# Kernel optimization log

Measured on AMD Instinct MI355X. Metric: run time of the kernel, lower is better.

The kernel has to match this reference:

```python
import jax, jax.numpy as jnp
import numpy as np

B, IN_LEN, L = 32, 10, 16384
N_POLY, M_MODES, K_STR, CH, NB = 12, 6, 2, 20, 4


def _legendre_filters():
    # Midpoints of n equal intervals on [-1, 1]
    j = np.arange(N_POLY)
    xs = -1.0 + (2.0 * j + 1.0) / N_POLY
    fr = np.stack([np.polynomial.legendre.Legendre.basis(i)(xs) for i in range(M_MODES)])
    fd = fr * ((2.0 * np.arange(M_MODES) + 1.0) / N_POLY)[:, None]  # decomposition quadrature weights
    return fd[:, None, :].astype(np.float32), fr[:, None, :].astype(np.float32)


def _conv1d(x, w, stride=1):
    return jax.lax.conv_general_dilated(x, w, (stride,), 'VALID',
                                        dimension_numbers=('NCH', 'OIH', 'NCH'))


def setup_inputs() -> dict:
    key = jax.random.key(0)
    ks = jax.random.split(key, 7)
    sc = 0.1
    fd, fr = _legendre_filters()
    return {
        'input':   jax.random.normal(ks[0], (B, IN_LEN, L), jnp.float32),
        'w_first': jax.random.normal(ks[1], (CH, IN_LEN, 3), jnp.float32) * sc,
        'conv_a':  jax.random.normal(ks[2], (NB, CH, CH, 3), jnp.float32) * sc,
        'conv_b':  jax.random.normal(ks[3], (NB, CH, CH, 3), jnp.float32) * sc,
        'lin_m':   jax.random.normal(ks[4], (NB, CH, M_MODES, M_MODES), jnp.float32) * sc,
        'w11':     jax.random.normal(ks[5], (128, CH, 1), jnp.float32) * sc,
        'w_out':   jax.random.normal(ks[6], (1, 128, 1), jnp.float32) * sc,
        'filt_d':  jnp.asarray(fd),
        'filt_r':  jnp.asarray(fr),
    }


def reference(input, w_first, conv_a, conv_b, lin_m, w11, w_out, filt_d, filt_r):
    n, m, kk = N_POLY, M_MODES, K_STR
    s = n // kk                      # conv stride = 6
    nb = conv_a.shape[0]
    RR = (n // kk) * (kk - 1)        # 6
    recept = RR * nb + 1
    rc = 2
    gelu = lambda t: jax.nn.gelu(t, approximate=False)

    b, _, Lin = input.shape
    li = Lin + 2 * recept - 2
    half = n // 2
    r = half - li % half             # circular padding to make strided conv exact
    x = jnp.pad(input, ((0, 0), (0, 0), (recept, recept + r)), mode='wrap')
    x = _conv1d(x, w_first)          # (b, CH, l)
    c = x.shape[1]

    for i in range(nb):
        l = x.shape[-1]
        # local residual branch: conv3 -> gelu -> conv3
        linear_x = _conv1d(gelu(_conv1d(x, conv_a[i])), conv_b[i])  # (b, c, l-4)
        # Legendre decomposition: strided conv per (b,c) signal
        xr = x.reshape(b * c, 1, l)
        Lx = _conv1d(xr, filt_d / kk, stride=s)                     # (b*c, m, ll)
        ll = Lx.shape[-1]
        Lx = Lx.reshape(b, c, m, ll).transpose(0, 2, 1, 3).reshape(b, m * c, ll)
        # grouped 1x1 conv: groups=c consecutive chunks of size m over the (mode-major) channel axis
        Lg = Lx.reshape(b, c, m, ll)
        Lg = jnp.einsum('bgil,goi->bgol', Lg, lin_m[i])
        Lx2 = Lg.reshape(b, m * c, ll)
        Lx2 = Lx2.reshape(b, m, c, ll).transpose(0, 2, 1, 3).reshape(b * c, m, ll) * 2.0
        # conv_transpose1d (stride s, kernel n=2s) via overlap-add of two half-kernels
        y = jnp.einsum('xmt,mk->xtk', Lx2, (filt_r / kk)[:, 0, :])  # (b*c, ll, n)
        p1 = y[..., :s].reshape(b * c, ll * s)
        p2 = y[..., s:].reshape(b * c, ll * s)
        rec = jnp.pad(p1, ((0, 0), (0, s))) + jnp.pad(p2, ((0, 0), (s, 0)))  # (b*c, l)
        rec = rec.reshape(b, c, l)
        x = gelu(rec[:, :, RR:-RR] + linear_x[:, :, RR - rc:-(RR - rc)])

    x = gelu(jnp.einsum('bcl,oc->bol', x, w11[:, :, 0]))
    x = jnp.einsum('bcl,oc->bol', x, w_out[:, :, 0])
    return x[:, :, :-r]
```

## Files before the change

kernel.cpp:

```cpp
#include <hip/hip_runtime.h>
#include <math.h>

#define B_ 32
#define INLEN 10
#define LIN_ 16384
#define NPOLY 12
#define MM 6
#define CH 20
#define NB 4
#define RECEPT 25
#define L0 16434
#define TTILE 252
#define NW 43
#define XS_LEN 264
#define XS_PAD 265
#define GS_LEN 254
#define LXS_PAD 121
#define CCHUNK 5
#define COH 10

__device__ __forceinline__ float gelu_exact(float x) {
    return 0.5f * x * (1.0f + erff(x * 0.70710678118654752440f));
}

__global__ void k_first(const float* __restrict__ in, const float* __restrict__ wf,
                        float* __restrict__ out) {
    int t = blockIdx.x * blockDim.x + threadIdx.x;
    int b = blockIdx.y;
    if (t >= L0) return;
    const float* inb = in + (size_t)b * INLEN * LIN_;
    float xw[INLEN][3];
#pragma unroll
    for (int ci = 0; ci < INLEN; ++ci) {
#pragma unroll
        for (int k = 0; k < 3; ++k) {
            int idx = t + k - RECEPT;
            idx = (idx < 0) ? idx + LIN_ : (idx >= LIN_ ? idx - LIN_ : idx);
            xw[ci][k] = inb[ci * LIN_ + idx];
        }
    }
    float* outb = out + (size_t)b * CH * L0;
#pragma unroll
    for (int co = 0; co < CH; ++co) {
        float acc = 0.f;
#pragma unroll
        for (int ci = 0; ci < INLEN; ++ci)
#pragma unroll
            for (int k = 0; k < 3; ++k)
                acc = fmaf(xw[ci][k], wf[(co * INLEN + ci) * 3 + k], acc);
        outb[(size_t)co * L0 + t] = acc;
    }
}

__global__ __launch_bounds__(512, 2)
void k_block(const float* __restrict__ x, float* __restrict__ xn,
             const float* __restrict__ wA, const float* __restrict__ wB,
             const float* __restrict__ linm, const float* __restrict__ fd,
             const float* __restrict__ fr, int l) {
    const int lout = l - 12;
    const int tid  = threadIdx.x;
    const int t    = tid & 255;
    const int half = __builtin_amdgcn_readfirstlane(tid >> 8);
    const int cob  = half * COH;
    const int t0   = blockIdx.x * TTILE;
    const int b    = blockIdx.y;

    const float* wAh = wA + cob * CH * 3;
    const float* wBh = wB + cob * CH * 3;

    __shared__ float xs[CH][XS_PAD];
    __shared__ float lxs[NW][LXS_PAD];
    __shared__ float lm_s[CH * MM * MM];
    __shared__ float fr_s[MM * NPOLY];

    const float* xb = x + (size_t)b * CH * l;

    for (int i = tid; i < CH * MM * MM; i += 512) lm_s[i] = linm[i];
    for (int i = tid; i < MM * NPOLY; i += 512)   fr_s[i] = fr[i];

    for (int i = tid; i < CH * XS_LEN; i += 512) {
        int c = i / XS_LEN, p = i - c * XS_LEN;
        int gp = t0 + p;
        xs[c][p] = (gp < l) ? xb[(size_t)c * l + gp] : 0.f;
    }
    __syncthreads();

    for (int item = tid; item < NW * CH; item += 512) {
        int wl = item / CH, c = item - wl * CH;
        float xv[NPOLY];
#pragma unroll
        for (int k = 0; k < NPOLY; ++k) xv[k] = xs[c][6 * wl + k];
#pragma unroll
        for (int m = 0; m < MM; ++m) {
            float acc = 0.f;
#pragma unroll
            for (int k = 0; k < NPOLY; ++k)
                acc = fmaf(xv[k], fd[m * NPOLY + k], acc);
            lxs[wl][m * CH + c] = acc * 0.5f;
        }
    }

    float gv[COH];
    if (t < GS_LEN) {
#pragma unroll
        for (int co = 0; co < COH; ++co) gv[co] = 0.f;
#pragma unroll 1
        for (int cig = 0; cig < CH; cig += CCHUNK) {
            float xw[CCHUNK][3];
#pragma unroll
            for (int j = 0; j < CCHUNK; ++j) {
                xw[j][0] = xs[cig + j][t + 4];
                xw[j][1] = xs[cig + j][t + 5];
                xw[j][2] = xs[cig + j][t + 6];
            }
#pragma unroll
            for (int co = 0; co < COH; ++co) {
                float acc = gv[co];
#pragma unroll
                for (int j = 0; j < CCHUNK; ++j)
#pragma unroll
                    for (int k = 0; k < 3; ++k)
                        acc = fmaf(xw[j][k], wAh[(co * CH + cig + j) * 3 + k], acc);
                gv[co] = acc;
            }
        }
#pragma unroll
        for (int co = 0; co < COH; ++co) gv[co] = gelu_exact(gv[co]);
    }
    __syncthreads();

    if (t < GS_LEN) {
#pragma unroll
        for (int co = 0; co < COH; ++co) xs[cob + co][t] = gv[co];
    }

    for (int item = tid; item < NW * CH; item += 512) {
        int wl = item / CH, g = item - wl * CH;
        float iv[MM], ov[MM];
#pragma unroll
        for (int i = 0; i < MM; ++i) iv[i] = lxs[wl][g * MM + i];
#pragma unroll
        for (int o = 0; o < MM; ++o) {
            float acc = 0.f;
#pragma unroll
            for (int i = 0; i < MM; ++i)
                acc = fmaf(iv[i], lm_s[(g * MM + o) * MM + i], acc);
            ov[o] = acc;
        }
#pragma unroll
        for (int o = 0; o < MM; ++o) lxs[wl][g * MM + o] = ov[o];
    }
    __syncthreads();

    if (t < TTILE && t0 + t < lout) {
        const int tp = t;
        float acc[COH];
#pragma unroll
        for (int co = 0; co < COH; ++co) acc[co] = 0.f;
#pragma unroll 1
        for (int cig = 0; cig < CH; cig += CCHUNK) {
            float aw[CCHUNK][3];
#pragma unroll
            for (int j = 0; j < CCHUNK; ++j) {
                aw[j][0] = xs[cig + j][tp];
                aw[j][1] = xs[cig + j][tp + 1];
                aw[j][2] = xs[cig + j][tp + 2];
            }
#pragma unroll
            for (int co = 0; co < COH; ++co) {
                float a = acc[co];
#pragma unroll
                for (int j = 0; j < CCHUNK; ++j)
#pragma unroll
                    for (int k = 0; k < 3; ++k)
                        a = fmaf(aw[j][k], wBh[(co * CH + cig + j) * 3 + k], a);
                acc[co] = a;
            }
        }
        const int r1  = tp % 6;
        const int wl1 = tp / 6 + 1;
        float frA[MM], frB[MM];
#pragma unroll
        for (int m = 0; m < MM; ++m) {
            frA[m] = fr_s[m * NPOLY + r1];
            frB[m] = fr_s[m * NPOLY + r1 + 6];
        }
        float* xnb = xn + (size_t)b * CH * lout + (size_t)cob * lout;
#pragma unroll
        for (int co = 0; co < COH; ++co) {
            float rec = 0.f;
#pragma unroll
            for (int m = 0; m < MM; ++m) {
                rec = fmaf(lxs[wl1][m * CH + cob + co], frA[m], rec);
                rec = fmaf(lxs[wl1 - 1][m * CH + cob + co], frB[m], rec);
            }
            xnb[(size_t)co * lout + t0 + tp] = gelu_exact(acc[co] + rec);
        }
    }
}

__global__ void k_final(const float* __restrict__ x, const float* __restrict__ w11,
                        const float* __restrict__ wout, float* __restrict__ out) {
    int t = blockIdx.x * blockDim.x + threadIdx.x;
    int b = blockIdx.y;
    if (t >= LIN_) return;
    const int l4 = L0 - NB * 12;
    const float* xb = x + (size_t)b * CH * l4;
    float xv[CH];
#pragma unroll
    for (int c = 0; c < CH; ++c) xv[c] = xb[(size_t)c * l4 + t];
    float acc0 = 0.f, acc1 = 0.f, acc2 = 0.f, acc3 = 0.f;
    for (int h = 0; h < 128; h += 4) {
        float hv0 = 0.f, hv1 = 0.f, hv2 = 0.f, hv3 = 0.f;
#pragma unroll
        for (int c = 0; c < CH; ++c) {
            hv0 = fmaf(xv[c], w11[(h + 0) * CH + c], hv0);
            hv1 = fmaf(xv[c], w11[(h + 1) * CH + c], hv1);
            hv2 = fmaf(xv[c], w11[(h + 2) * CH + c], hv2);
            hv3 = fmaf(xv[c], w11[(h + 3) * CH + c], hv3);
        }
        acc0 = fmaf(gelu_exact(hv0), wout[h + 0], acc0);
        acc1 = fmaf(gelu_exact(hv1), wout[h + 1], acc1);
        acc2 = fmaf(gelu_exact(hv2), wout[h + 2], acc2);
        acc3 = fmaf(gelu_exact(hv3), wout[h + 3], acc3);
    }
    out[(size_t)b * LIN_ + t] = (acc0 + acc1) + (acc2 + acc3);
}

extern "C" void kernel_launch(void* const* d_in, const int* in_sizes, int n_in,
                              void* d_out, int out_size, void* d_ws, size_t ws_size,
                              hipStream_t stream) {
    const float* input   = (const float*)d_in[0];
    const float* w_first = (const float*)d_in[1];
    const float* conv_a  = (const float*)d_in[2];
    const float* conv_b  = (const float*)d_in[3];
    const float* lin_m   = (const float*)d_in[4];
    const float* w11     = (const float*)d_in[5];
    const float* w_out   = (const float*)d_in[6];
    const float* filt_d  = (const float*)d_in[7];
    const float* filt_r  = (const float*)d_in[8];
    float* out = (float*)d_out;

    const size_t bufElems = (size_t)B_ * CH * L0;
    float* xA = (float*)d_ws;
    float* xB = xA + bufElems;

    {
        dim3 grid((L0 + 255) / 256, B_);
        k_first<<<grid, 256, 0, stream>>>(input, w_first, xA);
    }

    int l = L0;
    float* cur = xA;
    float* nxt = xB;
    for (int i = 0; i < NB; ++i) {
        int lout  = l - 12;
        int tiles = (lout + TTILE - 1) / TTILE;
        dim3 grid(tiles, B_);
        k_block<<<grid, 512, 0, stream>>>(cur, nxt,
                                          conv_a + i * CH * CH * 3,
                                          conv_b + i * CH * CH * 3,
                                          lin_m + i * CH * MM * MM,
                                          filt_d, filt_r, l);
        float* tswap = cur; cur = nxt; nxt = tswap;
        l = lout;
    }

    {
        dim3 grid((LIN_ + 255) / 256, B_);
        k_final<<<grid, 256, 0, stream>>>(cur, w11, w_out, out);
    }
}
```

Before: 495.3 us.

## Fuse first conv into first block and final MLP into last block

The stem convolution is computed inside the first residual-block kernel from a shared-memory tile of the wrapped input, and the last block kernel applies the 1x1 conv, GELU and output projection itself, splitting the 128 hidden units across the two thread halves. This removes two kernel launches and the global write and re-read of a full 20-channel activation tensor at each end. In exchange the first block recomputes the stem conv on tile halos, and the last block gains extra syncs and a serial 64-hidden loop per thread.

Result: no change. 487.1 us (-1.7%).

```diff
diff --git a/kernel.cpp b/kernel.cpp
--- a/kernel.cpp
+++ b/kernel.cpp
@@ -18,45 +18,21 @@
 #define LXS_PAD 121
 #define CCHUNK 5
 #define COH 10
+#define INW 266
 
 __device__ __forceinline__ float gelu_exact(float x) {
     return 0.5f * x * (1.0f + erff(x * 0.70710678118654752440f));
 }
 
-__global__ void k_first(const float* __restrict__ in, const float* __restrict__ wf,
-                        float* __restrict__ out) {
-    int t = blockIdx.x * blockDim.x + threadIdx.x;
-    int b = blockIdx.y;
-    if (t >= L0) return;
-    const float* inb = in + (size_t)b * INLEN * LIN_;
-    float xw[INLEN][3];
-#pragma unroll
-    for (int ci = 0; ci < INLEN; ++ci) {
-#pragma unroll
-        for (int k = 0; k < 3; ++k) {
-            int idx = t + k - RECEPT;
-            idx = (idx < 0) ? idx + LIN_ : (idx >= LIN_ ? idx - LIN_ : idx);
-            xw[ci][k] = inb[ci * LIN_ + idx];
-        }
-    }
-    float* outb = out + (size_t)b * CH * L0;
-#pragma unroll
-    for (int co = 0; co < CH; ++co) {
-        float acc = 0.f;
-#pragma unroll
-        for (int ci = 0; ci < INLEN; ++ci)
-#pragma unroll
-            for (int k = 0; k < 3; ++k)
-                acc = fmaf(xw[ci][k], wf[(co * INLEN + ci) * 3 + k], acc);
-        outb[(size_t)co * L0 + t] = acc;
-    }
-}
-
+template<int MODE>
 __global__ __launch_bounds__(512, 2)
 void k_block(const float* __restrict__ x, float* __restrict__ xn,
              const float* __restrict__ wA, const float* __restrict__ wB,
              const float* __restrict__ linm, const float* __restrict__ fd,
-             const float* __restrict__ fr, int l) {
+             const float* __restrict__ fr,
+             const float* __restrict__ in0, const float* __restrict__ wf,
+             const float* __restrict__ w11, const float* __restrict__ wout,
+             int l) {
     const int lout = l - 12;
     const int tid  = threadIdx.x;
     const int t    = tid & 255;
@@ -73,17 +49,58 @@
     __shared__ float lm_s[CH * MM * MM];
     __shared__ float fr_s[MM * NPOLY];
 
-    const float* xb = x + (size_t)b * CH * l;
-
     for (int i = tid; i < CH * MM * MM; i += 512) lm_s[i] = linm[i];
     for (int i = tid; i < MM * NPOLY; i += 512)   fr_s[i] = fr[i];
 
-    for (int i = tid; i < CH * XS_LEN; i += 512) {
-        int c = i / XS_LEN, p = i - c * XS_LEN;
-        int gp = t0 + p;
-        xs[c][p] = (gp < l) ? xb[(size_t)c * l + gp] : 0.f;
-    }
-    __syncthreads();
+    if constexpr (MODE == 0) {
+        float* inps = &lxs[0][0];
+        const float* inb = in0 + (size_t)b * INLEN * LIN_;
+        for (int i = tid; i < INLEN * INW; i += 512) {
+            int ci = i / INW, q = i - ci * INW;
+            int gq = t0 + q - RECEPT;
+            gq = (gq < 0) ? gq + LIN_ : (gq >= LIN_ ? gq - LIN_ : gq);
+            inps[i] = inb[(size_t)ci * LIN_ + gq];
+        }
+        __syncthreads();
+        const float* wfh = wf + cob * INLEN * 3;
+        for (int p = t; p < XS_LEN; p += 256) {
+            float acc[COH];
+#pragma unroll
+            for (int co = 0; co < COH; ++co) acc[co] = 0.f;
+#pragma unroll 1
+            for (int cig = 0; cig < INLEN; cig += CCHUNK) {
+                float xw[CCHUNK][3];
+#pragma unroll
+                for (int j = 0; j < CCHUNK; ++j) {
+                    xw[j][0] = inps[(cig + j) * INW + p];
+                    xw[j][1] = inps[(cig + j) * INW + p + 1];
+                    xw[j][2] = inps[(cig + j) * INW + p + 2];
+                }
+#pragma unroll
+                for (int co = 0; co < COH; ++co) {
+                    float a = acc[co];
+#pragma unroll
+                    for (int j = 0; j < CCHUNK; ++j)
+#pragma unroll
+                        for (int k = 0; k < 3; ++k)
+                            a = fmaf(xw[j][k], wfh[(co * INLEN + cig + j) * 3 + k], a);
+                    acc[co] = a;
+                }
+            }
+            const bool live = (t0 + p < l);
+#pragma unroll
+            for (int co = 0; co < COH; ++co) xs[cob + co][p] = live ? acc[co] : 0.f;
+        }
+        __syncthreads();
+    } else {
+        const float* xb = x + (size_t)b * CH * l;
+        for (int i = tid; i < CH * XS_LEN; i += 512) {
+            int c = i / XS_LEN, p = i - c * XS_LEN;
+            int gp = t0 + p;
+            xs[c][p] = (gp < l) ? xb[(size_t)c * l + gp] : 0.f;
+        }
+        __syncthreads();
+    }
 
     for (int item = tid; item < NW * CH; item += 512) {
         int wl = item / CH, c = item - wl * CH;
@@ -152,7 +169,9 @@
     }
     __syncthreads();
 
-    if (t < TTILE && t0 + t < lout) {
+    const bool vd = (t < TTILE) && (t0 + t < lout);
+    float outv[COH];
+    if (vd) {
         const int tp = t;
         float acc[COH];
 #pragma unroll
@@ -185,7 +204,6 @@
             frA[m] = fr_s[m * NPOLY + r1];
             frB[m] = fr_s[m * NPOLY + r1 + 6];
         }
-        float* xnb = xn + (size_t)b * CH * lout + (size_t)cob * lout;
 #pragma unroll
         for (int co = 0; co < COH; ++co) {
             float rec = 0.f;
@@ -194,37 +212,49 @@
                 rec = fmaf(lxs[wl1][m * CH + cob + co], frA[m], rec);
                 rec = fmaf(lxs[wl1 - 1][m * CH + cob + co], frB[m], rec);
             }
-            xnb[(size_t)co * lout + t0 + tp] = gelu_exact(acc[co] + rec);
-        }
-    }
-}
-
-__global__ void k_final(const float* __restrict__ x, const float* __restrict__ w11,
-                        const float* __restrict__ wout, float* __restrict__ out) {
-    int t = blockIdx.x * blockDim.x + threadIdx.x;
-    int b = blockIdx.y;
-    if (t >= LIN_) return;
-    const int l4 = L0 - NB * 12;
-    const float* xb = x + (size_t)b * CH * l4;
-    float xv[CH];
-#pragma unroll
-    for (int c = 0; c < CH; ++c) xv[c] = xb[(size_t)c * l4 + t];
-    float acc0 = 0.f, acc1 = 0.f, acc2 = 0.f, acc3 = 0.f;
-    for (int h = 0; h < 128; h += 4) {
-        float hv0 = 0.f, hv1 = 0.f, hv2 = 0.f, hv3 = 0.f;
-#pragma unroll
-        for (int c = 0; c < CH; ++c) {
-            hv0 = fmaf(xv[c], w11[(h + 0) * CH + c], hv0);
-            hv1 = fmaf(xv[c], w11[(h + 1) * CH + c], hv1);
-            hv2 = fmaf(xv[c], w11[(h + 2) * CH + c], hv2);
-            hv3 = fmaf(xv[c], w11[(h + 3) * CH + c], hv3);
-        }
-        acc0 = fmaf(gelu_exact(hv0), wout[h + 0], acc0);
-        acc1 = fmaf(gelu_exact(hv1), wout[h + 1], acc1);
-        acc2 = fmaf(gelu_exact(hv2), wout[h + 2], acc2);
-        acc3 = fmaf(gelu_exact(hv3), wout[h + 3], acc3);
-    }
-    out[(size_t)b * LIN_ + t] = (acc0 + acc1) + (acc2 + acc3);
+            outv[co] = gelu_exact(acc[co] + rec);
+        }
+        if constexpr (MODE != 2) {
+            float* xnb = xn + (size_t)b * CH * lout + (size_t)cob * lout;
+#pragma unroll
+            for (int co = 0; co < COH; ++co)
+                xnb[(size_t)co * lout + t0 + t] = outv[co];
+        }
+    }
+
+    if constexpr (MODE == 2) {
+        __syncthreads();
+        if (vd) {
+#pragma unroll
+            for (int co = 0; co < COH; ++co) xs[cob + co][t] = outv[co];
+        }
+        __syncthreads();
+        const bool vf = (t < TTILE) && (t0 + t < LIN_);
+        float* pb = &lxs[0][0];
+        if (vf) {
+            float xv[CH];
+#pragma unroll
+            for (int c = 0; c < CH; ++c) xv[c] = xs[c][t];
+            const float* w11h  = w11 + (size_t)(half * 64) * CH;
+            const float* wouth = wout + half * 64;
+            float partial = 0.f;
+#pragma unroll 1
+            for (int h = 0; h < 64; h += 2) {
+                float hv0 = 0.f, hv1 = 0.f;
+#pragma unroll
+                for (int c = 0; c < CH; ++c) {
+                    hv0 = fmaf(xv[c], w11h[h * CH + c], hv0);
+                    hv1 = fmaf(xv[c], w11h[(h + 1) * CH + c], hv1);
+                }
+                partial = fmaf(gelu_exact(hv0), wouth[h], partial);
+                partial = fmaf(gelu_exact(hv1), wouth[h + 1], partial);
+            }
+            pb[half * 256 + t] = partial;
+        }
+        __syncthreads();
+        if (vf && half == 0)
+            xn[(size_t)b * LIN_ + t0 + t] = pb[t] + pb[256 + t];
+    }
 }
 
 extern "C" void kernel_launch(void* const* d_in, const int* in_sizes, int n_in,
@@ -245,29 +275,31 @@
     float* xA = (float*)d_ws;
     float* xB = xA + bufElems;
 
+    const int WSTEP = CH * CH * 3;
+    const int MSTEP = CH * MM * MM;
+
     {
-        dim3 grid((L0 + 255) / 256, B_);
-        k_first<<<grid, 256, 0, stream>>>(input, w_first, xA);
-    }
-
-    int l = L0;
-    float* cur = xA;
-    float* nxt = xB;
-    for (int i = 0; i < NB; ++i) {
-        int lout  = l - 12;
-        int tiles = (lout + TTILE - 1) / TTILE;
-        dim3 grid(tiles, B_);
-        k_block<<<grid, 512, 0, stream>>>(cur, nxt,
-                                          conv_a + i * CH * CH * 3,
-                                          conv_b + i * CH * CH * 3,
-                                          lin_m + i * CH * MM * MM,
-                                          filt_d, filt_r, l);
-        float* tswap = cur; cur = nxt; nxt = tswap;
-        l = lout;
-    }
-
+        dim3 grid((L0 - 12 + TTILE - 1) / TTILE, B_);
+        k_block<0><<<grid, 512, 0, stream>>>(nullptr, xA, conv_a, conv_b, lin_m,
+                                             filt_d, filt_r, input, w_first,
+                                             nullptr, nullptr, L0);
+    }
     {
-        dim3 grid((LIN_ + 255) / 256, B_);
-        k_final<<<grid, 256, 0, stream>>>(cur, w11, w_out, out);
+        dim3 grid((L0 - 24 + TTILE - 1) / TTILE, B_);
+        k_block<1><<<grid, 512, 0, stream>>>(xA, xB, conv_a + WSTEP, conv_b + WSTEP,
+                                             lin_m + MSTEP, filt_d, filt_r,
+                                             nullptr, nullptr, nullptr, nullptr, L0 - 12);
+    }
+    {
+        dim3 grid((L0 - 36 + TTILE - 1) / TTILE, B_);
+        k_block<1><<<grid, 512, 0, stream>>>(xB, xA, conv_a + 2 * WSTEP, conv_b + 2 * WSTEP,
+                                             lin_m + 2 * MSTEP, filt_d, filt_r,
+                                             nullptr, nullptr, nullptr, nullptr, L0 - 24);
+    }
+    {
+        dim3 grid((LIN_ + TTILE - 1) / TTILE, B_);
+        k_block<2><<<grid, 512, 0, stream>>>(xA, out, conv_a + 3 * WSTEP, conv_b + 3 * WSTEP,
+                                             lin_m + 3 * MSTEP, filt_d, filt_r,
+                                             nullptr, nullptr, w11, w_out, L0 - 36);
     }
 }
```
